# Performance work log

Measured on AMD Instinct MI355X. Metric: run time of the kernel, lower is better.

Reference implementation:

```python
import jax, jax.numpy as jnp
import numpy as np

N = 50000      # num_nodes
E = 800000     # num_edges (before self-loops)
IN = 512       # in_channels
HID = 64       # hidden_channels
H = 8          # num_heads (layer 1)
OUT = 128      # out_channels
NEG_SLOPE = 0.2


def setup_inputs() -> dict:
    key = jax.random.key(0)
    ks = jax.random.split(key, 10)
    x = jax.random.normal(ks[0], (N, IN), jnp.float32)
    edge_index = jax.random.randint(ks[1], (2, E), 0, N, jnp.int32)

    def glorot(k, shape):
        fan_in, fan_out = shape[0], int(np.prod(shape[1:]))
        s = jnp.sqrt(2.0 / (fan_in + fan_out)).astype(jnp.float32)
        return jax.random.normal(k, shape, jnp.float32) * s

    # layer 1: GATConv(IN -> HID, heads=H, concat=True)
    W1 = glorot(ks[2], (IN, H * HID))
    att_src1 = glorot(ks[3], (H, HID))
    att_dst1 = glorot(ks[4], (H, HID))
    b1 = jnp.zeros((H * HID,), jnp.float32)
    # layer 2: GATConv(H*HID -> OUT, heads=1, concat=False)
    W2 = glorot(ks[5], (H * HID, OUT))
    att_src2 = glorot(ks[6], (1, OUT))
    att_dst2 = glorot(ks[7], (1, OUT))
    b2 = jnp.zeros((OUT,), jnp.float32)
    return {"x": x, "edge_index": edge_index,
            "W1": W1, "b1": b1, "att_src1": att_src1, "att_dst1": att_dst1,
            "W2": W2, "b2": b2, "att_src2": att_src2, "att_dst2": att_dst2}


def gat_layer(x, src, dst, W, b, a_src, a_dst, heads, concat):
    n = x.shape[0]
    h = (x @ W).reshape(n, heads, -1)                     # [N, H, C]
    e_src = (h * a_src).sum(-1)                           # [N, H]
    e_dst = (h * a_dst).sum(-1)                           # [N, H]
    e = jax.nn.leaky_relu(e_src[src] + e_dst[dst], NEG_SLOPE)   # [E, H]
    # segment softmax over incoming edges of each destination node
    m = jax.ops.segment_max(e, dst, num_segments=n)       # [N, H]
    m = jnp.where(jnp.isneginf(m), 0.0, m)                # empty segments
    p = jnp.exp(e - m[dst])                               # [E, H]
    s = jax.ops.segment_sum(p, dst, num_segments=n)       # [N, H]
    alpha = p / (s[dst] + 1e-16)                          # [E, H]
    out = jax.ops.segment_sum(alpha[..., None] * h[src], dst, num_segments=n)  # [N, H, C]
    if concat:
        return out.reshape(n, -1) + b
    return out.mean(axis=1) + b


def reference(x, edge_index, W1, b1, att_src1, att_dst1, W2, b2, att_src2, att_dst2):
    # PyG GATConv adds self-loops by default
    loops = jnp.arange(N, dtype=edge_index.dtype)
    src = jnp.concatenate([edge_index[0], loops])
    dst = jnp.concatenate([edge_index[1], loops])
    h = gat_layer(x, src, dst, W1, b1, att_src1, att_dst1, H, True)   # [N, H*HID]
    h = jax.nn.relu(h)
    out = gat_layer(h, src, dst, W2, b2, att_src2, att_dst2, 1, False)  # [N, OUT]
    return out
```

## Files before the change

### kernel.cpp

```cpp
#include <hip/hip_runtime.h>

#define NNODES 50000
#define NEDGES 800000
#define ETOT   (NNODES + NEDGES)
#define NH     8
#define HID    64
#define D1     512
#define INC    512
#define OUTC   128
#define NEG    0.2f
#define MPAD   50048

typedef __attribute__((ext_vector_type(8))) short short8;
typedef __attribute__((ext_vector_type(4))) float f32x4;

__device__ __forceinline__ float bf2f(ushort u) { return __uint_as_float(((uint)u) << 16); }
__device__ __forceinline__ ushort f2bf(float x) {
    uint u = __float_as_uint(x);
    u += 0x7fffu + ((u >> 16) & 1u);
    return (ushort)(u >> 16);
}
__device__ __forceinline__ float leaky(float v) { return v >= 0.f ? v : NEG * v; }

__global__ void count_deg(const int* __restrict__ ei, int* __restrict__ deg) {
    int i = blockIdx.x * 256 + threadIdx.x;
    if (i >= ETOT) return;
    int dst = (i < NEDGES) ? ei[NEDGES + i] : (i - NEDGES);
    atomicAdd(&deg[dst], 1);
}

__global__ void scan_deg(const int* __restrict__ deg, int* __restrict__ rs) {
    __shared__ int part[1024];
    const int n = NNODES;
    const int CH = (n + 1023) / 1024;
    int t = threadIdx.x;
    int lo = t * CH, hi = min(lo + CH, n);
    int s = 0;
    for (int i = lo; i < hi; ++i) s += deg[i];
    part[t] = s;
    __syncthreads();
    for (int off = 1; off < 1024; off <<= 1) {
        int v = (t >= off) ? part[t - off] : 0;
        __syncthreads();
        part[t] += v;
        __syncthreads();
    }
    int run = (t == 0) ? 0 : part[t - 1];
    for (int i = lo; i < hi; ++i) { rs[i] = run; run += deg[i]; }
    if (hi == n) rs[n] = run;
}

__global__ void scatter_edges(const int* __restrict__ ei, int* __restrict__ cursor,
                              int* __restrict__ csr_src) {
    int i = blockIdx.x * 256 + threadIdx.x;
    if (i >= ETOT) return;
    int src, dst;
    if (i < NEDGES) { src = ei[i]; dst = ei[NEDGES + i]; }
    else            { src = dst = i - NEDGES; }
    int pos = atomicAdd(&cursor[dst], 1);
    csr_src[pos] = src;
}

__global__ void cast_bf16(const float* __restrict__ x, ushort* __restrict__ xb, int n4) {
    int i = blockIdx.x * 256 + threadIdx.x;
    if (i >= n4) return;
    float4 v = *(const float4*)&x[(size_t)i * 4];
    ushort4 o = { f2bf(v.x), f2bf(v.y), f2bf(v.z), f2bf(v.w) };
    *(ushort4*)&xb[(size_t)i * 4] = o;
}

__global__ void cast_wT(const float* __restrict__ W, ushort* __restrict__ WT, int K, int N) {
    int idx = blockIdx.x * 256 + threadIdx.x;
    if (idx >= K * N) return;
    int n = idx / K, k = idx - n * K;
    WT[idx] = f2bf(W[(size_t)k * N + n]);
}

template<int KDIM>
__global__ __launch_bounds__(256) void gemm_bf16(const ushort* __restrict__ A,
                                                 const ushort* __restrict__ Bt,
                                                 ushort* __restrict__ C,
                                                 int M, int N) {
    __shared__ __align__(16) ushort Asl[128 * 64];
    __shared__ __align__(16) ushort Bsl[128 * 64];
    const int tid  = threadIdx.x;
    const int lane = tid & 63;
    const int wid  = tid >> 6;
    const int wr   = wid >> 1, wc = wid & 1;
    const int fr   = lane & 15, fq = lane >> 4;
    const int m0   = blockIdx.x * 128;
    const int n0   = blockIdx.y * 128;

    f32x4 acc[4][4] = {};

    for (int k0 = 0; k0 < KDIM; k0 += 64) {
        __syncthreads();
        #pragma unroll
        for (int i = 0; i < 4; ++i) {
            int chunk = wid * 4 + i;
            int r = chunk * 8 + (lane >> 3);
            const ushort* ga = A  + (size_t)(m0 + r) * KDIM + k0 + (lane & 7) * 8;
            const ushort* gb = Bt + (size_t)(n0 + r) * KDIM + k0 + (lane & 7) * 8;
            __builtin_amdgcn_global_load_lds(
                (const __attribute__((address_space(1))) void*)ga,
                (__attribute__((address_space(3))) void*)(Asl + chunk * 512), 16, 0, 0);
            __builtin_amdgcn_global_load_lds(
                (const __attribute__((address_space(1))) void*)gb,
                (__attribute__((address_space(3))) void*)(Bsl + chunk * 512), 16, 0, 0);
        }
        __syncthreads();
        #pragma unroll
        for (int ks = 0; ks < 2; ++ks) {
            short8 a[4], b[4];
            #pragma unroll
            for (int m = 0; m < 4; ++m)
                a[m] = *(const short8*)&Asl[(wr * 64 + m * 16 + fr) * 64 + ks * 32 + fq * 8];
            #pragma unroll
            for (int n = 0; n < 4; ++n)
                b[n] = *(const short8*)&Bsl[(wc * 64 + n * 16 + fr) * 64 + ks * 32 + fq * 8];
            #pragma unroll
            for (int m = 0; m < 4; ++m)
                #pragma unroll
                for (int n = 0; n < 4; ++n)
                    acc[m][n] = __builtin_amdgcn_mfma_f32_16x16x32_bf16(a[m], b[n], acc[m][n], 0, 0, 0);
        }
    }
    #pragma unroll
    for (int m = 0; m < 4; ++m) {
        #pragma unroll
        for (int r = 0; r < 4; ++r) {
            int row = m0 + wr * 64 + m * 16 + fq * 4 + r;
            if (row >= M) continue;
            #pragma unroll
            for (int n = 0; n < 4; ++n)
                C[(size_t)row * N + n0 + wc * 64 + n * 16 + fr] = f2bf(acc[m][n][r]);
        }
    }
}

__global__ void dots1(const ushort* __restrict__ h1, const float* __restrict__ a_src,
                      const float* __restrict__ a_dst,
                      float* __restrict__ es, float* __restrict__ ed) {
    int gw   = (blockIdx.x * blockDim.x + threadIdx.x) >> 6;
    int lane = threadIdx.x & 63;
    if (gw >= NNODES) return;
    short8 v = *(const short8*)&h1[(size_t)gw * D1 + lane * 8];
    int h = lane >> 3, c0 = (lane & 7) * 8;
    float s = 0.f, d = 0.f;
    #pragma unroll
    for (int j = 0; j < 8; ++j) {
        float x = bf2f((ushort)v[j]);
        s += x * a_src[h * HID + c0 + j];
        d += x * a_dst[h * HID + c0 + j];
    }
    #pragma unroll
    for (int off = 1; off < 8; off <<= 1) {
        s += __shfl_xor(s, off);
        d += __shfl_xor(d, off);
    }
    if ((lane & 7) == 0) { es[gw * NH + h] = s; ed[gw * NH + h] = d; }
}

__global__ void dots2(const ushort* __restrict__ h2, const float* __restrict__ a_src,
                      const float* __restrict__ a_dst,
                      float* __restrict__ es, float* __restrict__ ed) {
    int gw   = (blockIdx.x * blockDim.x + threadIdx.x) >> 6;
    int lane = threadIdx.x & 63;
    if (gw >= NNODES) return;
    uint u = *(const uint*)&h2[(size_t)gw * OUTC + lane * 2];
    float x0 = bf2f((ushort)(u & 0xffffu)), x1 = bf2f((ushort)(u >> 16));
    float s = x0 * a_src[lane * 2] + x1 * a_src[lane * 2 + 1];
    float d = x0 * a_dst[lane * 2] + x1 * a_dst[lane * 2 + 1];
    #pragma unroll
    for (int off = 1; off < 64; off <<= 1) {
        s += __shfl_xor(s, off);
        d += __shfl_xor(d, off);
    }
    if (lane == 0) { es[gw] = s; ed[gw] = d; }
}

#define CAP1 128
__global__ __launch_bounds__(256) void attn1(const ushort* __restrict__ h1,
                                             const float* __restrict__ esrc,
                                             const float* __restrict__ edst,
                                             const int* __restrict__ rs,
                                             const int* __restrict__ csr_src,
                                             const float* __restrict__ b1,
                                             ushort* __restrict__ out1) {
    int n = blockIdx.x;
    int t = threadIdx.x;
    int lane = t & 63, wid = t >> 6;
    int beg = rs[n], deg = rs[n + 1] - beg;
    int dcap = min(deg, CAP1);
    __shared__ float alpha_sh[NH][CAP1];
    __shared__ int   ssrc_sh[CAP1];
    __shared__ float msh[NH], rinv_sh[NH];

    for (int e = t; e < dcap; e += 256) ssrc_sh[e] = csr_src[beg + e];
    __syncthreads();

    {
        int h0 = wid * 2;
        float edn0 = edst[n * NH + h0], edn1 = edst[n * NH + h0 + 1];
        float m0 = -1e30f, m1 = -1e30f;
        for (int e = lane; e < deg; e += 64) {
            int s = (e < CAP1) ? ssrc_sh[e] : csr_src[beg + e];
            float2 es2 = *(const float2*)&esrc[s * NH + h0];
            float v0 = leaky(es2.x + edn0), v1 = leaky(es2.y + edn1);
            if (e < CAP1) { alpha_sh[h0][e] = v0; alpha_sh[h0 + 1][e] = v1; }
            m0 = fmaxf(m0, v0); m1 = fmaxf(m1, v1);
        }
        #pragma unroll
        for (int off = 32; off; off >>= 1) {
            m0 = fmaxf(m0, __shfl_xor(m0, off));
            m1 = fmaxf(m1, __shfl_xor(m1, off));
        }
        float s0 = 0.f, s1 = 0.f;
        for (int e = lane; e < deg; e += 64) {
            float v0, v1;
            if (e < CAP1) { v0 = alpha_sh[h0][e]; v1 = alpha_sh[h0 + 1][e]; }
            else {
                int s = csr_src[beg + e];
                float2 es2 = *(const float2*)&esrc[s * NH + h0];
                v0 = leaky(es2.x + edn0); v1 = leaky(es2.y + edn1);
            }
            float p0 = __expf(v0 - m0), p1 = __expf(v1 - m1);
            if (e < CAP1) { alpha_sh[h0][e] = p0; alpha_sh[h0 + 1][e] = p1; }
            s0 += p0; s1 += p1;
        }
        #pragma unroll
        for (int off = 32; off; off >>= 1) {
            s0 += __shfl_xor(s0, off);
            s1 += __shfl_xor(s1, off);
        }
        if (lane == 0) {
            msh[h0] = m0; msh[h0 + 1] = m1;
            rinv_sh[h0] = 1.f / (s0 + 1e-16f);
            rinv_sh[h0 + 1] = 1.f / (s1 + 1e-16f);
        }
    }
    __syncthreads();

    int c0 = 2 * t;
    int h = t >> 5;
    float m = msh[h], ri = rinv_sh[h];
    float edn = edst[n * NH + h];
    float acc0 = 0.f, acc1 = 0.f;
    int e = 0;
    for (; e + 4 <= dcap; e += 4) {
        int s0i = ssrc_sh[e], s1i = ssrc_sh[e + 1], s2i = ssrc_sh[e + 2], s3i = ssrc_sh[e + 3];
        uint u0 = *(const uint*)&h1[(size_t)s0i * D1 + c0];
        uint u1 = *(const uint*)&h1[(size_t)s1i * D1 + c0];
        uint u2 = *(const uint*)&h1[(size_t)s2i * D1 + c0];
        uint u3 = *(const uint*)&h1[(size_t)s3i * D1 + c0];
        float a0 = alpha_sh[h][e], a1 = alpha_sh[h][e + 1];
        float a2 = alpha_sh[h][e + 2], a3 = alpha_sh[h][e + 3];
        acc0 += a0 * bf2f((ushort)(u0 & 0xffffu)) + a1 * bf2f((ushort)(u1 & 0xffffu))
              + a2 * bf2f((ushort)(u2 & 0xffffu)) + a3 * bf2f((ushort)(u3 & 0xffffu));
        acc1 += a0 * bf2f((ushort)(u0 >> 16)) + a1 * bf2f((ushort)(u1 >> 16))
              + a2 * bf2f((ushort)(u2 >> 16)) + a3 * bf2f((ushort)(u3 >> 16));
    }
    for (; e < dcap; ++e) {
        int s = ssrc_sh[e];
        float a = alpha_sh[h][e];
        uint u = *(const uint*)&h1[(size_t)s * D1 + c0];
        acc0 += a * bf2f((ushort)(u & 0xffffu));
        acc1 += a * bf2f((ushort)(u >> 16));
    }
    for (; e < deg; ++e) {
        int s = csr_src[beg + e];
        float a = __expf(leaky(esrc[s * NH + h] + edn) - m);
        uint u = *(const uint*)&h1[(size_t)s * D1 + c0];
        acc0 += a * bf2f((ushort)(u & 0xffffu));
        acc1 += a * bf2f((ushort)(u >> 16));
    }
    float o0 = fmaxf(acc0 * ri + b1[c0], 0.f);
    float o1 = fmaxf(acc1 * ri + b1[c0 + 1], 0.f);
    uint pk = (uint)f2bf(o0) | ((uint)f2bf(o1) << 16);
    *(uint*)&out1[(size_t)n * D1 + c0] = pk;
}

#define CAP2 128
__global__ __launch_bounds__(256) void attn2(const ushort* __restrict__ h2,
                                             const float* __restrict__ esrc,
                                             const float* __restrict__ edst,
                                             const int* __restrict__ rs,
                                             const int* __restrict__ csr_src,
                                             const float* __restrict__ b2,
                                             float* __restrict__ out) {
    int lane = threadIdx.x & 63, wid = threadIdx.x >> 6;
    int n = blockIdx.x * 4 + wid;
    if (n >= NNODES) return;
    int beg = rs[n], deg = rs[n + 1] - beg;
    int dcap = min(deg, CAP2);
    __shared__ float al_sh[4][CAP2];
    __shared__ int   ss_sh[4][CAP2];
    float* al = al_sh[wid];
    int*   ss = ss_sh[wid];

    for (int e = lane; e < dcap; e += 64) ss[e] = csr_src[beg + e];

    float edn = edst[n];
    float m = -1e30f;
    for (int e = lane; e < deg; e += 64) {
        int s = (e < CAP2) ? ss[e] : csr_src[beg + e];
        float v = leaky(esrc[s] + edn);
        if (e < CAP2) al[e] = v;
        m = fmaxf(m, v);
    }
    #pragma unroll
    for (int off = 32; off; off >>= 1) m = fmaxf(m, __shfl_xor(m, off));
    float ssum = 0.f;
    for (int e = lane; e < deg; e += 64) {
        float v = (e < CAP2) ? al[e] : leaky(esrc[csr_src[beg + e]] + edn);
        float p = __expf(v - m);
        if (e < CAP2) al[e] = p;
        ssum += p;
    }
    #pragma unroll
    for (int off = 32; off; off >>= 1) ssum += __shfl_xor(ssum, off);
    float ri = 1.f / (ssum + 1e-16f);

    int c0 = 2 * lane;
    float acc0 = 0.f, acc1 = 0.f;
    int e = 0;
    for (; e + 4 <= dcap; e += 4) {
        int s0i = ss[e], s1i = ss[e + 1], s2i = ss[e + 2], s3i = ss[e + 3];
        uint u0 = *(const uint*)&h2[(size_t)s0i * OUTC + c0];
        uint u1 = *(const uint*)&h2[(size_t)s1i * OUTC + c0];
        uint u2 = *(const uint*)&h2[(size_t)s2i * OUTC + c0];
        uint u3 = *(const uint*)&h2[(size_t)s3i * OUTC + c0];
        float a0 = al[e], a1 = al[e + 1], a2 = al[e + 2], a3 = al[e + 3];
        acc0 += a0 * bf2f((ushort)(u0 & 0xffffu)) + a1 * bf2f((ushort)(u1 & 0xffffu))
              + a2 * bf2f((ushort)(u2 & 0xffffu)) + a3 * bf2f((ushort)(u3 & 0xffffu));
        acc1 += a0 * bf2f((ushort)(u0 >> 16)) + a1 * bf2f((ushort)(u1 >> 16))
              + a2 * bf2f((ushort)(u2 >> 16)) + a3 * bf2f((ushort)(u3 >> 16));
    }
    for (; e < dcap; ++e) {
        int s = ss[e];
        float a = al[e];
        uint u = *(const uint*)&h2[(size_t)s * OUTC + c0];
        acc0 += a * bf2f((ushort)(u & 0xffffu));
        acc1 += a * bf2f((ushort)(u >> 16));
    }
    for (; e < deg; ++e) {
        int s = csr_src[beg + e];
        float a = __expf(leaky(esrc[s] + edn) - m);
        uint u = *(const uint*)&h2[(size_t)s * OUTC + c0];
        acc0 += a * bf2f((ushort)(u & 0xffffu));
        acc1 += a * bf2f((ushort)(u >> 16));
    }
    float2 o = { acc0 * ri + b2[c0], acc1 * ri + b2[c0 + 1] };
    *(float2*)&out[(size_t)n * OUTC + c0] = o;
}

extern "C" void kernel_launch(void* const* d_in, const int* in_sizes, int n_in,
                              void* d_out, int out_size, void* d_ws, size_t ws_size,
                              hipStream_t stream) {
    const float* x   = (const float*)d_in[0];
    const int*   ei  = (const int*)  d_in[1];
    const float* W1  = (const float*)d_in[2];
    const float* b1  = (const float*)d_in[3];
    const float* as1 = (const float*)d_in[4];
    const float* ad1 = (const float*)d_in[5];
    const float* W2  = (const float*)d_in[6];
    const float* b2  = (const float*)d_in[7];
    const float* as2 = (const float*)d_in[8];
    const float* ad2 = (const float*)d_in[9];
    float* out = (float*)d_out;

    char* ws = (char*)d_ws;
    size_t off = 0;
    auto alloc = [&](size_t bytes) -> void* {
        void* p = ws + off;
        off = (off + bytes + 255) & ~(size_t)255;
        return p;
    };
    ushort* xb    = (ushort*)alloc((size_t)MPAD * INC * 2);
    ushort* w1t   = (ushort*)alloc((size_t)D1 * INC * 2);
    ushort* w2t   = (ushort*)alloc((size_t)OUTC * D1 * 2);
    ushort* h1b   = (ushort*)alloc((size_t)MPAD * D1 * 2);
    ushort* out1b = (ushort*)alloc((size_t)MPAD * D1 * 2);
    ushort* h2b   = (ushort*)alloc((size_t)MPAD * OUTC * 2);
    float*  es1   = (float*)alloc((size_t)NNODES * NH * 4);
    float*  ed1   = (float*)alloc((size_t)NNODES * NH * 4);
    float*  es2   = (float*)alloc((size_t)NNODES * 4);
    float*  ed2   = (float*)alloc((size_t)NNODES * 4);
    int*    deg   = (int*)alloc((size_t)NNODES * 4);
    int*    rs    = (int*)alloc((size_t)(NNODES + 1) * 4);
    int*    cur   = (int*)alloc((size_t)NNODES * 4);
    int*    csr   = (int*)alloc((size_t)ETOT * 4);

    hipMemsetAsync(deg, 0, (size_t)NNODES * 4, stream);
    count_deg<<<(ETOT + 255) / 256, 256, 0, stream>>>(ei, deg);
    scan_deg<<<1, 1024, 0, stream>>>(deg, rs);
    hipMemcpyAsync(cur, rs, (size_t)NNODES * 4, hipMemcpyDeviceToDevice, stream);
    scatter_edges<<<(ETOT + 255) / 256, 256, 0, stream>>>(ei, cur, csr);

    cast_bf16<<<(NNODES * INC / 4 + 255) / 256, 256, 0, stream>>>(x, xb, NNODES * INC / 4);
    cast_wT<<<(INC * D1 + 255) / 256, 256, 0, stream>>>(W1, w1t, INC, D1);
    cast_wT<<<(D1 * OUTC + 255) / 256, 256, 0, stream>>>(W2, w2t, D1, OUTC);

    gemm_bf16<INC><<<dim3(MPAD / 128, D1 / 128), 256, 0, stream>>>(xb, w1t, h1b, NNODES, D1);
    dots1<<<(NNODES * 64 + 255) / 256, 256, 0, stream>>>(h1b, as1, ad1, es1, ed1);
    attn1<<<NNODES, 256, 0, stream>>>(h1b, es1, ed1, rs, csr, b1, out1b);

    gemm_bf16<D1><<<dim3(MPAD / 128, OUTC / 128), 256, 0, stream>>>(out1b, w2t, h2b, NNODES, OUTC);
    dots2<<<(NNODES * 64 + 255) / 256, 256, 0, stream>>>(h2b, as2, ad2, es2, ed2);
    attn2<<<(NNODES + 3) / 4, 256, 0, stream>>>(h2b, es2, ed2, rs, csr, b2, out);
}
```

Before: 611.4 us.

## Switch intermediates to fp16 with packed half2 FMA aggregation and denser node blocks

Replaces bf16 storage with fp16 throughout (casts, MFMA f16 GEMM, intermediate features). The aggregation loops now use packed half2 FMAs on unnormalized attention weights stored as splatted half2 in shared memory. attn1 handles two nodes per block with 4 channels per thread, and attn2 uses 32-lane groups handling 8 nodes per block with wider loads. The aim is to cut ALU conversion work and raise memory-level parallelism in the gather kernels. The cost is fp16 range and precision risk: the unnormalized sums are accumulated in half, and large inputs or accumulations could overflow.

Measured after the change: 591.2 us. 3.3% less time.

```diff
diff --git a/kernel.cpp b/kernel.cpp
--- a/kernel.cpp
+++ b/kernel.cpp
@@ -1,4 +1,5 @@
 #include <hip/hip_runtime.h>
+#include <hip/hip_fp16.h>
 
 #define NNODES 50000
 #define NEDGES 800000
@@ -13,13 +14,19 @@
 
 typedef __attribute__((ext_vector_type(8))) short short8;
 typedef __attribute__((ext_vector_type(4))) float f32x4;
-
-__device__ __forceinline__ float bf2f(ushort u) { return __uint_as_float(((uint)u) << 16); }
-__device__ __forceinline__ ushort f2bf(float x) {
-    uint u = __float_as_uint(x);
-    u += 0x7fffu + ((u >> 16) & 1u);
-    return (ushort)(u >> 16);
-}
+typedef _Float16 half8v __attribute__((ext_vector_type(8)));
+typedef _Float16 half2v __attribute__((ext_vector_type(2)));
+
+__device__ __forceinline__ ushort f2h_bits(float x) {
+    _Float16 h = (_Float16)x; return __builtin_bit_cast(ushort, h);
+}
+__device__ __forceinline__ float h2f(ushort b) {
+    return (float)__builtin_bit_cast(_Float16, b);
+}
+__device__ __forceinline__ uint splat_h2(float p) {
+    uint b = (uint)f2h_bits(p); return b | (b << 16);
+}
+__device__ __forceinline__ half2v as_h2(uint u) { return __builtin_bit_cast(half2v, u); }
 __device__ __forceinline__ float leaky(float v) { return v >= 0.f ? v : NEG * v; }
 
 __global__ void count_deg(const int* __restrict__ ei, int* __restrict__ deg) {
@@ -61,26 +68,26 @@
     csr_src[pos] = src;
 }
 
-__global__ void cast_bf16(const float* __restrict__ x, ushort* __restrict__ xb, int n4) {
+__global__ void cast_f16(const float* __restrict__ x, ushort* __restrict__ xh, int n4) {
     int i = blockIdx.x * 256 + threadIdx.x;
     if (i >= n4) return;
     float4 v = *(const float4*)&x[(size_t)i * 4];
-    ushort4 o = { f2bf(v.x), f2bf(v.y), f2bf(v.z), f2bf(v.w) };
-    *(ushort4*)&xb[(size_t)i * 4] = o;
+    ushort4 o = { f2h_bits(v.x), f2h_bits(v.y), f2h_bits(v.z), f2h_bits(v.w) };
+    *(ushort4*)&xh[(size_t)i * 4] = o;
 }
 
 __global__ void cast_wT(const float* __restrict__ W, ushort* __restrict__ WT, int K, int N) {
     int idx = blockIdx.x * 256 + threadIdx.x;
     if (idx >= K * N) return;
     int n = idx / K, k = idx - n * K;
-    WT[idx] = f2bf(W[(size_t)k * N + n]);
+    WT[idx] = f2h_bits(W[(size_t)k * N + n]);
 }
 
 template<int KDIM>
-__global__ __launch_bounds__(256) void gemm_bf16(const ushort* __restrict__ A,
-                                                 const ushort* __restrict__ Bt,
-                                                 ushort* __restrict__ C,
-                                                 int M, int N) {
+__global__ __launch_bounds__(256) void gemm_f16(const ushort* __restrict__ A,
+                                                const ushort* __restrict__ Bt,
+                                                ushort* __restrict__ C,
+                                                int M, int N) {
     __shared__ __align__(16) ushort Asl[128 * 64];
     __shared__ __align__(16) ushort Bsl[128 * 64];
     const int tid  = threadIdx.x;
@@ -122,7 +129,9 @@
             for (int m = 0; m < 4; ++m)
                 #pragma unroll
                 for (int n = 0; n < 4; ++n)
-                    acc[m][n] = __builtin_amdgcn_mfma_f32_16x16x32_bf16(a[m], b[n], acc[m][n], 0, 0, 0);
+                    acc[m][n] = __builtin_amdgcn_mfma_f32_16x16x32_f16(
+                        __builtin_bit_cast(half8v, a[m]),
+                        __builtin_bit_cast(half8v, b[n]), acc[m][n], 0, 0, 0);
         }
     }
     #pragma unroll
@@ -133,7 +142,7 @@
             if (row >= M) continue;
             #pragma unroll
             for (int n = 0; n < 4; ++n)
-                C[(size_t)row * N + n0 + wc * 64 + n * 16 + fr] = f2bf(acc[m][n][r]);
+                C[(size_t)row * N + n0 + wc * 64 + n * 16 + fr] = f2h_bits(acc[m][n][r]);
         }
     }
 }
@@ -145,11 +154,12 @@
     int lane = threadIdx.x & 63;
     if (gw >= NNODES) return;
     short8 v = *(const short8*)&h1[(size_t)gw * D1 + lane * 8];
+    half8v hv = __builtin_bit_cast(half8v, v);
     int h = lane >> 3, c0 = (lane & 7) * 8;
     float s = 0.f, d = 0.f;
     #pragma unroll
     for (int j = 0; j < 8; ++j) {
-        float x = bf2f((ushort)v[j]);
+        float x = (float)hv[j];
         s += x * a_src[h * HID + c0 + j];
         d += x * a_dst[h * HID + c0 + j];
     }
@@ -168,7 +178,7 @@
     int lane = threadIdx.x & 63;
     if (gw >= NNODES) return;
     uint u = *(const uint*)&h2[(size_t)gw * OUTC + lane * 2];
-    float x0 = bf2f((ushort)(u & 0xffffu)), x1 = bf2f((ushort)(u >> 16));
+    float x0 = h2f((ushort)(u & 0xffffu)), x1 = h2f((ushort)(u >> 16));
     float s = x0 * a_src[lane * 2] + x1 * a_src[lane * 2 + 1];
     float d = x0 * a_dst[lane * 2] + x1 * a_dst[lane * 2 + 1];
     #pragma unroll
@@ -187,97 +197,132 @@
                                              const int* __restrict__ csr_src,
                                              const float* __restrict__ b1,
                                              ushort* __restrict__ out1) {
-    int n = blockIdx.x;
     int t = threadIdx.x;
     int lane = t & 63, wid = t >> 6;
+    int nidx = wid >> 1, wv = wid & 1;
+    int n = blockIdx.x * 2 + nidx;
     int beg = rs[n], deg = rs[n + 1] - beg;
     int dcap = min(deg, CAP1);
-    __shared__ float alpha_sh[NH][CAP1];
-    __shared__ int   ssrc_sh[CAP1];
-    __shared__ float msh[NH], rinv_sh[NH];
-
-    for (int e = t; e < dcap; e += 256) ssrc_sh[e] = csr_src[beg + e];
+    __shared__ float alpha_sh[2][CAP1][NH];
+    __shared__ int   ssrc_sh[2][CAP1];
+    __shared__ float msh[2][NH], rinv_sh[2][NH];
+
+    {
+        int e0 = t & 127;
+        for (int e = e0; e < dcap; e += 128) ssrc_sh[nidx][e] = csr_src[beg + e];
+    }
     __syncthreads();
 
     {
-        int h0 = wid * 2;
-        float edn0 = edst[n * NH + h0], edn1 = edst[n * NH + h0 + 1];
-        float m0 = -1e30f, m1 = -1e30f;
+        int h0 = wv * 4;
+        float4 ed4 = *(const float4*)&edst[n * NH + h0];
+        float m0 = -1e30f, m1 = -1e30f, m2 = -1e30f, m3 = -1e30f;
         for (int e = lane; e < deg; e += 64) {
-            int s = (e < CAP1) ? ssrc_sh[e] : csr_src[beg + e];
-            float2 es2 = *(const float2*)&esrc[s * NH + h0];
-            float v0 = leaky(es2.x + edn0), v1 = leaky(es2.y + edn1);
-            if (e < CAP1) { alpha_sh[h0][e] = v0; alpha_sh[h0 + 1][e] = v1; }
+            int s = (e < CAP1) ? ssrc_sh[nidx][e] : csr_src[beg + e];
+            float4 es4 = *(const float4*)&esrc[s * NH + h0];
+            float v0 = leaky(es4.x + ed4.x), v1 = leaky(es4.y + ed4.y);
+            float v2 = leaky(es4.z + ed4.z), v3 = leaky(es4.w + ed4.w);
+            if (e < CAP1) {
+                float4 vv = { v0, v1, v2, v3 };
+                *(float4*)&alpha_sh[nidx][e][h0] = vv;
+            }
             m0 = fmaxf(m0, v0); m1 = fmaxf(m1, v1);
+            m2 = fmaxf(m2, v2); m3 = fmaxf(m3, v3);
         }
         #pragma unroll
         for (int off = 32; off; off >>= 1) {
             m0 = fmaxf(m0, __shfl_xor(m0, off));
             m1 = fmaxf(m1, __shfl_xor(m1, off));
-        }
-        float s0 = 0.f, s1 = 0.f;
+            m2 = fmaxf(m2, __shfl_xor(m2, off));
+            m3 = fmaxf(m3, __shfl_xor(m3, off));
+        }
+        float s0 = 0.f, s1 = 0.f, s2 = 0.f, s3 = 0.f;
         for (int e = lane; e < deg; e += 64) {
-            float v0, v1;
-            if (e < CAP1) { v0 = alpha_sh[h0][e]; v1 = alpha_sh[h0 + 1][e]; }
-            else {
+            float v0, v1, v2, v3;
+            if (e < CAP1) {
+                float4 vv = *(const float4*)&alpha_sh[nidx][e][h0];
+                v0 = vv.x; v1 = vv.y; v2 = vv.z; v3 = vv.w;
+            } else {
                 int s = csr_src[beg + e];
-                float2 es2 = *(const float2*)&esrc[s * NH + h0];
-                v0 = leaky(es2.x + edn0); v1 = leaky(es2.y + edn1);
+                float4 es4 = *(const float4*)&esrc[s * NH + h0];
+                v0 = leaky(es4.x + ed4.x); v1 = leaky(es4.y + ed4.y);
+                v2 = leaky(es4.z + ed4.z); v3 = leaky(es4.w + ed4.w);
             }
             float p0 = __expf(v0 - m0), p1 = __expf(v1 - m1);
-            if (e < CAP1) { alpha_sh[h0][e] = p0; alpha_sh[h0 + 1][e] = p1; }
-            s0 += p0; s1 += p1;
+            float p2 = __expf(v2 - m2), p3 = __expf(v3 - m3);
+            if (e < CAP1) {
+                uint4 pk = { splat_h2(p0), splat_h2(p1), splat_h2(p2), splat_h2(p3) };
+                *(uint4*)&alpha_sh[nidx][e][h0] = pk;
+            }
+            s0 += p0; s1 += p1; s2 += p2; s3 += p3;
         }
         #pragma unroll
         for (int off = 32; off; off >>= 1) {
-            s0 += __shfl_xor(s0, off);
-            s1 += __shfl_xor(s1, off);
+            s0 += __shfl_xor(s0, off); s1 += __shfl_xor(s1, off);
+            s2 += __shfl_xor(s2, off); s3 += __shfl_xor(s3, off);
         }
         if (lane == 0) {
-            msh[h0] = m0; msh[h0 + 1] = m1;
-            rinv_sh[h0] = 1.f / (s0 + 1e-16f);
-            rinv_sh[h0 + 1] = 1.f / (s1 + 1e-16f);
+            msh[nidx][h0] = m0; msh[nidx][h0 + 1] = m1;
+            msh[nidx][h0 + 2] = m2; msh[nidx][h0 + 3] = m3;
+            rinv_sh[nidx][h0]     = 1.f / (s0 + 1e-16f);
+            rinv_sh[nidx][h0 + 1] = 1.f / (s1 + 1e-16f);
+            rinv_sh[nidx][h0 + 2] = 1.f / (s2 + 1e-16f);
+            rinv_sh[nidx][h0 + 3] = 1.f / (s3 + 1e-16f);
         }
     }
     __syncthreads();
 
-    int c0 = 2 * t;
-    int h = t >> 5;
-    float m = msh[h], ri = rinv_sh[h];
+    int tt = t & 127;
+    int c0 = tt * 4;
+    int h = tt >> 4;
+    float m = msh[nidx][h], ri = rinv_sh[nidx][h];
     float edn = edst[n * NH + h];
-    float acc0 = 0.f, acc1 = 0.f;
+    half2v a01 = {}, a01b = {}, a23 = {}, a23b = {};
+    const int* ss = ssrc_sh[nidx];
     int e = 0;
     for (; e + 4 <= dcap; e += 4) {
-        int s0i = ssrc_sh[e], s1i = ssrc_sh[e + 1], s2i = ssrc_sh[e + 2], s3i = ssrc_sh[e + 3];
-        uint u0 = *(const uint*)&h1[(size_t)s0i * D1 + c0];
-        uint u1 = *(const uint*)&h1[(size_t)s1i * D1 + c0];
-        uint u2 = *(const uint*)&h1[(size_t)s2i * D1 + c0];
-        uint u3 = *(const uint*)&h1[(size_t)s3i * D1 + c0];
-        float a0 = alpha_sh[h][e], a1 = alpha_sh[h][e + 1];
-        float a2 = alpha_sh[h][e + 2], a3 = alpha_sh[h][e + 3];
-        acc0 += a0 * bf2f((ushort)(u0 & 0xffffu)) + a1 * bf2f((ushort)(u1 & 0xffffu))
-              + a2 * bf2f((ushort)(u2 & 0xffffu)) + a3 * bf2f((ushort)(u3 & 0xffffu));
-        acc1 += a0 * bf2f((ushort)(u0 >> 16)) + a1 * bf2f((ushort)(u1 >> 16))
-              + a2 * bf2f((ushort)(u2 >> 16)) + a3 * bf2f((ushort)(u3 >> 16));
+        int s0i = ss[e], s1i = ss[e + 1], s2i = ss[e + 2], s3i = ss[e + 3];
+        uint2 u0 = *(const uint2*)&h1[(size_t)s0i * D1 + c0];
+        uint2 u1 = *(const uint2*)&h1[(size_t)s1i * D1 + c0];
+        uint2 u2 = *(const uint2*)&h1[(size_t)s2i * D1 + c0];
+        uint2 u3 = *(const uint2*)&h1[(size_t)s3i * D1 + c0];
+        half2v p0 = as_h2(*(const uint*)&alpha_sh[nidx][e][h]);
+        half2v p1 = as_h2(*(const uint*)&alpha_sh[nidx][e + 1][h]);
+        half2v p2 = as_h2(*(const uint*)&alpha_sh[nidx][e + 2][h]);
+        half2v p3 = as_h2(*(const uint*)&alpha_sh[nidx][e + 3][h]);
+        a01  = as_h2(u0.x) * p0 + a01;  a23  = as_h2(u0.y) * p0 + a23;
+        a01b = as_h2(u1.x) * p1 + a01b; a23b = as_h2(u1.y) * p1 + a23b;
+        a01  = as_h2(u2.x) * p2 + a01;  a23  = as_h2(u2.y) * p2 + a23;
+        a01b = as_h2(u3.x) * p3 + a01b; a23b = as_h2(u3.y) * p3 + a23b;
     }
     for (; e < dcap; ++e) {
-        int s = ssrc_sh[e];
-        float a = alpha_sh[h][e];
-        uint u = *(const uint*)&h1[(size_t)s * D1 + c0];
-        acc0 += a * bf2f((ushort)(u & 0xffffu));
-        acc1 += a * bf2f((ushort)(u >> 16));
+        int s = ss[e];
+        uint2 u = *(const uint2*)&h1[(size_t)s * D1 + c0];
+        half2v p = as_h2(*(const uint*)&alpha_sh[nidx][e][h]);
+        a01 = as_h2(u.x) * p + a01;
+        a23 = as_h2(u.y) * p + a23;
     }
     for (; e < deg; ++e) {
         int s = csr_src[beg + e];
-        float a = __expf(leaky(esrc[s * NH + h] + edn) - m);
-        uint u = *(const uint*)&h1[(size_t)s * D1 + c0];
-        acc0 += a * bf2f((ushort)(u & 0xffffu));
-        acc1 += a * bf2f((ushort)(u >> 16));
-    }
-    float o0 = fmaxf(acc0 * ri + b1[c0], 0.f);
-    float o1 = fmaxf(acc1 * ri + b1[c0 + 1], 0.f);
-    uint pk = (uint)f2bf(o0) | ((uint)f2bf(o1) << 16);
-    *(uint*)&out1[(size_t)n * D1 + c0] = pk;
+        float p = __expf(leaky(esrc[s * NH + h] + edn) - m);
+        half2v ph = as_h2(splat_h2(p));
+        uint2 u = *(const uint2*)&h1[(size_t)s * D1 + c0];
+        a01 = as_h2(u.x) * ph + a01;
+        a23 = as_h2(u.y) * ph + a23;
+    }
+    float ac0 = (float)a01[0] + (float)a01b[0];
+    float ac1 = (float)a01[1] + (float)a01b[1];
+    float ac2 = (float)a23[0] + (float)a23b[0];
+    float ac3 = (float)a23[1] + (float)a23b[1];
+    float4 bb = *(const float4*)&b1[c0];
+    float o0 = fmaxf(ac0 * ri + bb.x, 0.f);
+    float o1 = fmaxf(ac1 * ri + bb.y, 0.f);
+    float o2 = fmaxf(ac2 * ri + bb.z, 0.f);
+    float o3 = fmaxf(ac3 * ri + bb.w, 0.f);
+    uint2 pkout;
+    pkout.x = (uint)f2h_bits(o0) | ((uint)f2h_bits(o1) << 16);
+    pkout.y = (uint)f2h_bits(o2) | ((uint)f2h_bits(o3) << 16);
+    *(uint2*)&out1[(size_t)n * D1 + c0] = pkout;
 }
 
 #define CAP2 128
@@ -288,70 +333,80 @@
                                              const int* __restrict__ csr_src,
                                              const float* __restrict__ b2,
                                              float* __restrict__ out) {
-    int lane = threadIdx.x & 63, wid = threadIdx.x >> 6;
-    int n = blockIdx.x * 4 + wid;
+    int t = threadIdx.x;
+    int g = t >> 5, lane32 = t & 31;
+    int n = blockIdx.x * 8 + g;
     if (n >= NNODES) return;
     int beg = rs[n], deg = rs[n + 1] - beg;
     int dcap = min(deg, CAP2);
-    __shared__ float al_sh[4][CAP2];
-    __shared__ int   ss_sh[4][CAP2];
-    float* al = al_sh[wid];
-    int*   ss = ss_sh[wid];
-
-    for (int e = lane; e < dcap; e += 64) ss[e] = csr_src[beg + e];
+    __shared__ float al_sh[8][CAP2];
+    __shared__ int   ss_sh[8][CAP2];
+    float* al = al_sh[g];
+    int*   ss = ss_sh[g];
+
+    for (int e = lane32; e < dcap; e += 32) ss[e] = csr_src[beg + e];
 
     float edn = edst[n];
     float m = -1e30f;
-    for (int e = lane; e < deg; e += 64) {
+    for (int e = lane32; e < deg; e += 32) {
         int s = (e < CAP2) ? ss[e] : csr_src[beg + e];
         float v = leaky(esrc[s] + edn);
         if (e < CAP2) al[e] = v;
         m = fmaxf(m, v);
     }
     #pragma unroll
-    for (int off = 32; off; off >>= 1) m = fmaxf(m, __shfl_xor(m, off));
+    for (int off = 16; off; off >>= 1) m = fmaxf(m, __shfl_xor(m, off));
     float ssum = 0.f;
-    for (int e = lane; e < deg; e += 64) {
+    for (int e = lane32; e < deg; e += 32) {
         float v = (e < CAP2) ? al[e] : leaky(esrc[csr_src[beg + e]] + edn);
         float p = __expf(v - m);
-        if (e < CAP2) al[e] = p;
+        if (e < CAP2) *(uint*)&al[e] = splat_h2(p);
         ssum += p;
     }
     #pragma unroll
-    for (int off = 32; off; off >>= 1) ssum += __shfl_xor(ssum, off);
+    for (int off = 16; off; off >>= 1) ssum += __shfl_xor(ssum, off);
     float ri = 1.f / (ssum + 1e-16f);
 
-    int c0 = 2 * lane;
-    float acc0 = 0.f, acc1 = 0.f;
+    int c0 = lane32 * 4;
+    half2v a01 = {}, a01b = {}, a23 = {}, a23b = {};
     int e = 0;
     for (; e + 4 <= dcap; e += 4) {
         int s0i = ss[e], s1i = ss[e + 1], s2i = ss[e + 2], s3i = ss[e + 3];
-        uint u0 = *(const uint*)&h2[(size_t)s0i * OUTC + c0];
-        uint u1 = *(const uint*)&h2[(size_t)s1i * OUTC + c0];
-        uint u2 = *(const uint*)&h2[(size_t)s2i * OUTC + c0];
-        uint u3 = *(const uint*)&h2[(size_t)s3i * OUTC + c0];
-        float a0 = al[e], a1 = al[e + 1], a2 = al[e + 2], a3 = al[e + 3];
-        acc0 += a0 * bf2f((ushort)(u0 & 0xffffu)) + a1 * bf2f((ushort)(u1 & 0xffffu))
-              + a2 * bf2f((ushort)(u2 & 0xffffu)) + a3 * bf2f((ushort)(u3 & 0xffffu));
-        acc1 += a0 * bf2f((ushort)(u0 >> 16)) + a1 * bf2f((ushort)(u1 >> 16))
-              + a2 * bf2f((ushort)(u2 >> 16)) + a3 * bf2f((ushort)(u3 >> 16));
+        uint2 u0 = *(const uint2*)&h2[(size_t)s0i * OUTC + c0];
+        uint2 u1 = *(const uint2*)&h2[(size_t)s1i * OUTC + c0];
+        uint2 u2 = *(const uint2*)&h2[(size_t)s2i * OUTC + c0];
+        uint2 u3 = *(const uint2*)&h2[(size_t)s3i * OUTC + c0];
+        half2v p0 = as_h2(*(const uint*)&al[e]);
+        half2v p1 = as_h2(*(const uint*)&al[e + 1]);
+        half2v p2 = as_h2(*(const uint*)&al[e + 2]);
+        half2v p3 = as_h2(*(const uint*)&al[e + 3]);
+        a01  = as_h2(u0.x) * p0 + a01;  a23  = as_h2(u0.y) * p0 + a23;
+        a01b = as_h2(u1.x) * p1 + a01b; a23b = as_h2(u1.y) * p1 + a23b;
+        a01  = as_h2(u2.x) * p2 + a01;  a23  = as_h2(u2.y) * p2 + a23;
+        a01b = as_h2(u3.x) * p3 + a01b; a23b = as_h2(u3.y) * p3 + a23b;
     }
     for (; e < dcap; ++e) {
         int s = ss[e];
-        float a = al[e];
-        uint u = *(const uint*)&h2[(size_t)s * OUTC + c0];
-        acc0 += a * bf2f((ushort)(u & 0xffffu));
-        acc1 += a * bf2f((ushort)(u >> 16));
+        uint2 u = *(const uint2*)&h2[(size_t)s * OUTC + c0];
+        half2v p = as_h2(*(const uint*)&al[e]);
+        a01 = as_h2(u.x) * p + a01;
+        a23 = as_h2(u.y) * p + a23;
     }
     for (; e < deg; ++e) {
         int s = csr_src[beg + e];
-        float a = __expf(leaky(esrc[s] + edn) - m);
-        uint u = *(const uint*)&h2[(size_t)s * OUTC + c0];
-        acc0 += a * bf2f((ushort)(u & 0xffffu));
-        acc1 += a * bf2f((ushort)(u >> 16));
-    }
-    float2 o = { acc0 * ri + b2[c0], acc1 * ri + b2[c0 + 1] };
-    *(float2*)&out[(size_t)n * OUTC + c0] = o;
+        float p = __expf(leaky(esrc[s] + edn) - m);
+        half2v ph = as_h2(splat_h2(p));
+        uint2 u = *(const uint2*)&h2[(size_t)s * OUTC + c0];
+        a01 = as_h2(u.x) * ph + a01;
+        a23 = as_h2(u.y) * ph + a23;
+    }
+    float4 bb = *(const float4*)&b2[c0];
+    float4 o;
+    o.x = ((float)a01[0] + (float)a01b[0]) * ri + bb.x;
+    o.y = ((float)a01[1] + (float)a01b[1]) * ri + bb.y;
+    o.z = ((float)a23[0] + (float)a23b[0]) * ri + bb.z;
+    o.w = ((float)a23[1] + (float)a23b[1]) * ri + bb.w;
+    *(float4*)&out[(size_t)n * OUTC + c0] = o;
 }
 
 extern "C" void kernel_launch(void* const* d_in, const int* in_sizes, int n_in,
@@ -376,12 +431,12 @@
         off = (off + bytes + 255) & ~(size_t)255;
         return p;
     };
-    ushort* xb    = (ushort*)alloc((size_t)MPAD * INC * 2);
+    ushort* xh    = (ushort*)alloc((size_t)MPAD * INC * 2);
     ushort* w1t   = (ushort*)alloc((size_t)D1 * INC * 2);
     ushort* w2t   = (ushort*)alloc((size_t)OUTC * D1 * 2);
-    ushort* h1b   = (ushort*)alloc((size_t)MPAD * D1 * 2);
-    ushort* out1b = (ushort*)alloc((size_t)MPAD * D1 * 2);
-    ushort* h2b   = (ushort*)alloc((size_t)MPAD * OUTC * 2);
+    ushort* h1h   = (ushort*)alloc((size_t)MPAD * D1 * 2);
+    ushort* out1h = (ushort*)alloc((size_t)MPAD * D1 * 2);
+    ushort* h2h   = (ushort*)alloc((size_t)MPAD * OUTC * 2);
     float*  es1   = (float*)alloc((size_t)NNODES * NH * 4);
     float*  ed1   = (float*)alloc((size_t)NNODES * NH * 4);
     float*  es2   = (float*)alloc((size_t)NNODES * 4);
@@ -397,15 +452,15 @@
     hipMemcpyAsync(cur, rs, (size_t)NNODES * 4, hipMemcpyDeviceToDevice, stream);
     scatter_edges<<<(ETOT + 255) / 256, 256, 0, stream>>>(ei, cur, csr);
 
-    cast_bf16<<<(NNODES * INC / 4 + 255) / 256, 256, 0, stream>>>(x, xb, NNODES * INC / 4);
+    cast_f16<<<(NNODES * INC / 4 + 255) / 256, 256, 0, stream>>>(x, xh, NNODES * INC / 4);
     cast_wT<<<(INC * D1 + 255) / 256, 256, 0, stream>>>(W1, w1t, INC, D1);
     cast_wT<<<(D1 * OUTC + 255) / 256, 256, 0, stream>>>(W2, w2t, D1, OUTC);
 
-    gemm_bf16<INC><<<dim3(MPAD / 128, D1 / 128), 256, 0, stream>>>(xb, w1t, h1b, NNODES, D1);
-    dots1<<<(NNODES * 64 + 255) / 256, 256, 0, stream>>>(h1b, as1, ad1, es1, ed1);
-    attn1<<<NNODES, 256, 0, stream>>>(h1b, es1, ed1, rs, csr, b1, out1b);
-
-    gemm_bf16<D1><<<dim3(MPAD / 128, OUTC / 128), 256, 0, stream>>>(out1b, w2t, h2b, NNODES, OUTC);
-    dots2<<<(NNODES * 64 + 255) / 256, 256, 0, stream>>>(h2b, as2, ad2, es2, ed2);
-    attn2<<<(NNODES + 3) / 4, 256, 0, stream>>>(h2b, es2, ed2, rs, csr, b2, out);
-}
+    gemm_f16<INC><<<dim3(MPAD / 128, D1 / 128), 256, 0, stream>>>(xh, w1t, h1h, NNODES, D1);
+    dots1<<<(NNODES * 64 + 255) / 256, 256, 0, stream>>>(h1h, as1, ad1, es1, ed1);
+    attn1<<<NNODES / 2, 256, 0, stream>>>(h1h, es1, ed1, rs, csr, b1, out1h);
+
+    gemm_f16<D1><<<dim3(MPAD / 128, OUTC / 128), 256, 0, stream>>>(out1h, w2t, h2h, NNODES, OUTC);
+    dots2<<<(NNODES * 64 + 255) / 256, 256, 0, stream>>>(h2h, as2, ad2, es2, ed2);
+    attn2<<<NNODES / 8, 256, 0, stream>>>(h2h, es2, ed2, rs, csr, b2, out);
+}
```
